# Optimization experiments

Hardware: AMD Instinct MI355X
Metric: run time of the kernel (lower is better)

Reference implementation:

```python
import jax, jax.numpy as jnp
import numpy as np
from jax import lax

B, T, F, C = 2, 249, 64, 256   # fixed by alpha/beta weight shapes in build()
K = 3                          # conv kernel size
FILT = 256                     # q/k conv filters (both blocks)
V = 256                        # v conv filters (both blocks)
OUT_CH = 64                    # conv2d_final filters (hardcoded)


def conv2d(x, w, b):
    # NHWC 'same' conv, stride 1, dilation 1
    return lax.conv_general_dilated(
        x, w, window_strides=(1, 1), padding='SAME',
        dimension_numbers=('NHWC', 'HWIO', 'NHWC')) + b


def attn_block(x, wq, bq, wk, bk, wv, bv):
    # x: [B, H, L, C]; attention over L per (batch, H) slice
    q = conv2d(x, wq, bq)          # [B,H,L,FILT]
    k = conv2d(x, wk, bk)          # [B,H,L,FILT]
    v = conv2d(x, wv, bv)          # [B,H,L,V]
    scores = jnp.einsum('bhqc,bhkc->bhqk', q, k)   # [B,H,L,L]
    dist = jax.nn.softmax(scores, axis=-1)
    return jnp.einsum('bhqk,bhkc->bhqc', dist, v)  # [B,H,L,V]


def setup_inputs() -> dict:
    key = jax.random.key(0)
    ks = jax.random.split(key, 18)
    s = 0.05
    d = {'x': jax.random.normal(ks[0], (B, T, F, C), jnp.float32)}
    names = ['wq_f', 'wk_f', 'wv_f', 'wq_t', 'wk_t', 'wv_t']
    outs = [FILT, FILT, V, FILT, FILT, V]
    for i, (n, o) in enumerate(zip(names, outs)):
        d[n] = jax.random.normal(ks[1 + i], (K, K, C, o), jnp.float32) * s
        d['b' + n[1:]] = jnp.zeros((o,), jnp.float32)
    d['w_final'] = jax.random.normal(ks[8], (K, K, V + V + C, OUT_CH), jnp.float32) * s
    d['b_final'] = jnp.zeros((OUT_CH,), jnp.float32)
    d['alpha'] = jax.random.uniform(ks[9], (B, T, F, V), jnp.float32, -0.05, 0.05)
    d['beta'] = jax.random.uniform(ks[10], (B, T, F, V), jnp.float32, -0.05, 0.05)
    return d


def reference(x, wq_f, bq_f, wk_f, bk_f, wv_f, bv_f,
              wq_t, bq_t, wk_t, bk_t, wv_t, bv_t,
              w_final, b_final, alpha, beta):
    # AFAB: transpose to [B,F,T,C], attend over time axis T
    xt = jnp.transpose(x, (0, 2, 1, 3))
    out_freq = attn_block(xt, wq_f, bq_f, wk_f, bk_f, wv_f, bv_f)
    out_freq = jnp.transpose(out_freq, (0, 2, 1, 3))  # back to [B,T,F,V]
    # ATAB: attend over frequency axis F directly on [B,T,F,C]
    out_time = attn_block(x, wq_t, bq_t, wk_t, bk_t, wv_t, bv_t)
    # learned elementwise gating + concat + final conv (concatenation=True path)
    fused = jnp.concatenate([alpha * out_freq, beta * out_time, x], axis=-1)
    return conv2d(fused, w_final, b_final)
```

## Files before the change

kernel.cpp:

```cpp
#include <hip/hip_runtime.h>


typedef _Float16 f16;
typedef _Float16 f16x8 __attribute__((ext_vector_type(8)));
typedef float    f32x4 __attribute__((ext_vector_type(4)));

#define B_   2
#define T_   249
#define F_   64
#define TP   251
#define FP   66
#define PIXB (T_*F_)
#define NPIX (B_*PIXB)
#define LPAD 256
#define XPOS (B_*TP*FP)

static constexpr size_t FUSED_BYTES = (size_t)B_*TP*FP*768*2;
static constexpr size_t XPAD_BYTES  = (size_t)B_*TP*FP*256*2;
static constexpr size_t QF_BYTES    = (size_t)B_*64*LPAD*256*2;
static constexpr size_t QT_BYTES    = (size_t)B_*T_*64*256*2;
static constexpr size_t WT_BYTES    = (size_t)9*1536*256*2;
static constexpr size_t WFT_BYTES   = (size_t)9*64*768*2;

static constexpr size_t OFF_FUSED = 0;
static constexpr size_t OFF_XPAD  = OFF_FUSED + FUSED_BYTES;
static constexpr size_t OFF_QF    = OFF_XPAD  + XPAD_BYTES;
static constexpr size_t OFF_KF    = OFF_QF + QF_BYTES;
static constexpr size_t OFF_VF    = OFF_KF + QF_BYTES;
static constexpr size_t OFF_QT    = OFF_VF + QF_BYTES;
static constexpr size_t OFF_KT    = OFF_QT + QT_BYTES;
static constexpr size_t OFF_VT    = OFF_KT + QT_BYTES;
static constexpr size_t OFF_WT    = OFF_VT + QT_BYTES;
static constexpr size_t OFF_WFT   = OFF_WT + WT_BYTES;
static constexpr size_t OFF_BALL  = OFF_WFT + WFT_BYTES;
static constexpr size_t OFF_BF    = OFF_BALL + 1536*4;
static constexpr size_t WS_NEED   = OFF_BF + 64*4;

__device__ __forceinline__ f32x4 mfma16(f16x8 a, f16x8 b, f32x4 c) {
    return __builtin_amdgcn_mfma_f32_16x16x32_f16(a, b, c, 0, 0, 0);
}

__device__ __forceinline__ void gl_lds16(const void* g, void* l) {
    __builtin_amdgcn_global_load_lds(
        (const __attribute__((address_space(1))) unsigned int*)(unsigned long long)g,
        (__attribute__((address_space(3))) unsigned int*)(unsigned int)(unsigned long long)l,
        16, 0, 0);
}

__global__ __launch_bounds__(256) void prep_w(
    const float* __restrict__ wqf, const float* __restrict__ wkf, const float* __restrict__ wvf,
    const float* __restrict__ wqt, const float* __restrict__ wkt, const float* __restrict__ wvt,
    const float* __restrict__ wfin,
    const float* __restrict__ bqf, const float* __restrict__ bkf, const float* __restrict__ bvf,
    const float* __restrict__ bqt, const float* __restrict__ bkt, const float* __restrict__ bvt,
    const float* __restrict__ bfin,
    f16* __restrict__ wT, f16* __restrict__ wfT,
    float* __restrict__ biasAll, float* __restrict__ biasF)
{
    int idx = blockIdx.x*256 + threadIdx.x;
    if (idx < 9*1536*256) {
        int tap = idx / (1536*256);
        int r   = idx - tap*(1536*256);
        int n = r >> 8, c = r & 255;
        int dt = tap/3 - 1, df = tap%3 - 1;
        int blk = n >> 8, nl = n & 255;
        const float* w; int kh, kw;
        if (blk < 3) { w = (blk==0) ? wqf : (blk==1) ? wkf : wvf; kh = df+1; kw = dt+1; }
        else         { w = (blk==3) ? wqt : (blk==4) ? wkt : wvt; kh = dt+1; kw = df+1; }
        wT[idx] = (f16)w[((kh*3 + kw)*256 + c)*256 + nl];
    }
    if (idx < 9*64*768) {
        int tap = idx / (64*768);
        int r   = idx - tap*(64*768);
        int oc = r / 768, cin = r - oc*768;
        int dt = tap/3 - 1, df = tap%3 - 1;
        wfT[idx] = (f16)wfin[(((dt+1)*3 + (df+1))*768 + cin)*64 + oc];
    }
    if (idx < 1536) {
        int blk = idx >> 8, nl = idx & 255;
        const float* bb = (blk==0)?bqf:(blk==1)?bkf:(blk==2)?bvf:(blk==3)?bqt:(blk==4)?bkt:bvt;
        biasAll[idx] = bb[nl];
    }
    if (idx < 64) biasF[idx] = bfin[idx];
}

__global__ __launch_bounds__(256) void prep_x(
    const float* __restrict__ x, f16* __restrict__ xpad, f16* __restrict__ fused)
{
    int tid = blockIdx.x*256 + threadIdx.x;
    int pix = tid >> 5, c8 = (tid & 31)*8;
    int b = pix / PIXB; int r = pix - b*PIXB;
    int t = r >> 6, f = r & 63;
    const float* src = x + (size_t)pix*256 + c8;
    f16x8 v;
#pragma unroll
    for (int j = 0; j < 8; ++j) v[j] = (f16)src[j];
    size_t pp = (size_t)(b*TP + t + 1)*FP + (f + 1);
    *(f16x8*)(xpad + pp*256 + c8) = v;
    *(f16x8*)(fused + pp*768 + 512 + c8) = v;
}

__global__ __launch_bounds__(256) void border_zero(
    f16* __restrict__ xpad, f16* __restrict__ fused)
{
    int pix = blockIdx.x*2 + (threadIdx.x >> 7);
    int tl = threadIdx.x & 127;
    int b = pix / 630; int i = pix - b*630;
    int tp, fp;
    if (i < 66)       { tp = 0;   fp = i; }
    else if (i < 132) { tp = 250; fp = i - 66; }
    else { int j = i - 132; tp = 1 + (j >> 1); fp = (j & 1) * 65; }
    size_t pp = (size_t)(b*TP + tp)*FP + fp;
    f16x8 z = {0, 0, 0, 0, 0, 0, 0, 0};
    if (tl < 32) *(f16x8*)(xpad + pp*256 + tl*8) = z;
    if (tl < 96) *(f16x8*)(fused + pp*768 + tl*8) = z;
}

__global__ __launch_bounds__(512, 2) void conv_qkv(
    const f16* __restrict__ xpad, const f16* __restrict__ wT,
    const float* __restrict__ biasAll,
    f16* __restrict__ qf, f16* __restrict__ kf, f16* __restrict__ vf,
    f16* __restrict__ qt, f16* __restrict__ kt_, f16* __restrict__ vt)
{
    __shared__ f16 smemH[448*64];
    __shared__ f16 smemB[2][256*64];

    const int xcd = blockIdx.x & 7, lin = blockIdx.x >> 3;
    const int mtcnt = (xcd < 6) ? 16 : 15;
    if (lin >= 6*mtcnt) return;
    const int mtbase = (xcd < 6) ? xcd*16 : 96 + (xcd - 6)*15;
    const int nt = lin / mtcnt;
    const int mt = mtbase + (lin - nt*mtcnt);

    const int bb_ = mt / 63;
    const int t0  = (mt - bb_*63) * 4;
    const int Gs66 = (bb_*TP + t0) * 66;

    const int l   = threadIdx.x & 63;
    const int wid = threadIdx.x >> 6;
    const int wm = wid >> 2, wn = wid & 3;

    int hOff[7];
#pragma unroll
    for (int j = 0; j < 7; ++j) {
        int pos = j*64 + wid*8 + (l >> 3);
        int ps = pos;
        if (ps > 395) ps = 395;
        int pmax = (XPOS - 1) - Gs66/1;
        { int pm = XPOS - 1 - (bb_*TP + t0)*66; if (ps > pm) ps = pm; }
        (void)pmax;
        int ch = (l & 7) ^ (ps & 7);
        hOff[j] = (Gs66 + ps)*256 + ch*8;
    }
    int bSrc[4];
#pragma unroll
    for (int j = 0; j < 4; ++j) {
        int row = j*64 + wid*8 + (l >> 3);
        int ch = (l & 7) ^ (row & 7);
        bSrc[j] = (nt*256 + row)*256 + ch*8;
    }

    int pos00[8];
#pragma unroll
    for (int m = 0; m < 8; ++m) {
        int r = wm*128 + m*16 + (l & 15);
        pos00[m] = ((r >> 6) + 1)*66 + (r & 63) + 1;
    }
    int bRow[4], bSw[4];
#pragma unroll
    for (int n = 0; n < 4; ++n) {
        int row = wn*64 + n*16 + (l & 15);
        bRow[n] = row*64; bSw[n] = row & 7;
    }

    f32x4 acc[8][4];
#pragma unroll
    for (int m = 0; m < 8; ++m)
#pragma unroll
        for (int n = 0; n < 4; ++n) acc[m][n] = {0.f, 0.f, 0.f, 0.f};

#define HSTAGE(C) do {                                                         \
        _Pragma("unroll")                                                      \
        for (int j_ = 0; j_ < 7; ++j_)                                         \
            gl_lds16(xpad + hOff[j_] + (C)*64,                                 \
                     smemH + (j_*512 + wid*64)*8);                             \
    } while (0)

#define BSTAGE(TAP, C, NB) do {                                                \
        const f16* wt_ = wT + (size_t)(TAP)*(1536*256) + (C)*64;               \
        _Pragma("unroll")                                                      \
        for (int j_ = 0; j_ < 4; ++j_)                                         \
            gl_lds16(wt_ + bSrc[j_], &smemB[NB][(j_*512 + wid*64)*8]);         \
    } while (0)

#define QCOMP(NB, TAPOFF) do {                                                 \
        int pos_[8];                                                           \
        _Pragma("unroll")                                                      \
        for (int m = 0; m < 8; ++m) pos_[m] = pos00[m] + (TAPOFF);             \
        _Pragma("unroll")                                                      \
        for (int kk = 0; kk < 2; ++kk) {                                       \
            const int cch = kk*4 + (l >> 4);                                   \
            f16x8 af[8], bf[4];                                                \
            _Pragma("unroll")                                                  \
            for (int m = 0; m < 8; ++m)                                        \
                af[m] = *(const f16x8*)(smemH + pos_[m]*64 + ((cch ^ (pos_[m] & 7)) << 3)); \
            _Pragma("unroll")                                                  \
            for (int n = 0; n < 4; ++n)                                        \
                bf[n] = *(const f16x8*)(&smemB[NB][0] + bRow[n] + ((cch ^ bSw[n]) << 3)); \
            __builtin_amdgcn_s_setprio(1);                                     \
            _Pragma("unroll")                                                  \
            for (int m = 0; m < 8; ++m)                                        \
                _Pragma("unroll")                                              \
                for (int n = 0; n < 4; ++n)                                    \
                    acc[m][n] = mfma16(af[m], bf[n], acc[m][n]);               \
            __builtin_amdgcn_s_setprio(0);                                     \
        }                                                                      \
    } while (0)

    int buf = 0;
    HSTAGE(0);
    BSTAGE(0, 0, 0);
    __syncthreads();
    for (int c = 0; c < 4; ++c) {
        for (int tap = 0; tap < 9; ++tap) {
            if (tap < 8)      BSTAGE(tap + 1, c, buf ^ 1);
            else if (c < 3)   BSTAGE(0, c + 1, buf ^ 1);
            const int dt = tap/3 - 1, df = tap - (tap/3)*3 - 1;
            QCOMP(buf, dt*66 + df);
            __syncthreads();
            buf ^= 1;
        }
        if (c < 3) {
            HSTAGE(c + 1);
            __syncthreads();
        }
    }
#undef HSTAGE
#undef BSTAGE
#undef QCOMP

    f16* dst = (nt==0)?qf:(nt==1)?kf:(nt==2)?vf:(nt==3)?qt:(nt==4)?kt_:vt;
#pragma unroll
    for (int m = 0; m < 8; ++m) {
#pragma unroll
        for (int rg = 0; rg < 4; ++rg) {
            int row = wm*128 + m*16 + (l >> 4)*4 + rg;
            int t = t0 + (row >> 6), f = row & 63;
            if (t <= 248) {
#pragma unroll
                for (int n = 0; n < 4; ++n) {
                    int col = wn*64 + n*16 + (l & 15);
                    float v = acc[m][n][rg] + biasAll[nt*256 + col];
                    int off;
                    if (nt < 2)       off = ((bb_*64 + f)*LPAD + t)*256 + col;
                    else if (nt == 2) off = ((bb_*64 + f)*256 + col)*LPAD + t;
                    else if (nt < 5)  off = ((bb_*T_ + t)*64 + f)*256 + col;
                    else              off = ((bb_*T_ + t)*256 + col)*64 + f;
                    dst[off] = (f16)v;
                }
            }
        }
    }
}

__global__ __launch_bounds__(256) void attn_f(
    const f16* __restrict__ qf, const f16* __restrict__ kf, const f16* __restrict__ vf,
    const float* __restrict__ alpha, f16* __restrict__ fused)
{
    __shared__ f16 plds[4][16*256];
    const int l = threadIdx.x & 63;
    const int wid = threadIdx.x >> 6;
    const int head = blockIdx.x >> 2;
    const int qb = blockIdx.x & 3;
    const int b = head >> 6, f = head & 63;
    const f16* qh = qf + (size_t)head*LPAD*256;
    const f16* kh = kf + (size_t)head*LPAD*256;
    const f16* vh = vf + (size_t)head*256*LPAD;
    const int qr0 = qb*64 + wid*16;
    f16* pw = &plds[wid][0];

    f16x8 qa[8];
#pragma unroll
    for (int ks = 0; ks < 8; ++ks)
        qa[ks] = *(const f16x8*)(qh + (qr0 + (l & 15))*256 + ks*32 + (l >> 4)*8);

    f32x4 s[16];
#pragma unroll
    for (int nf = 0; nf < 16; ++nf) s[nf] = {0.f, 0.f, 0.f, 0.f};
#pragma unroll
    for (int ks = 0; ks < 8; ++ks)
#pragma unroll
        for (int nf = 0; nf < 16; ++nf) {
            f16x8 bf = *(const f16x8*)(kh + (nf*16 + (l & 15))*256 + ks*32 + (l >> 4)*8);
            s[nf] = mfma16(qa[ks], bf, s[nf]);
        }

    float inv[4];
#pragma unroll
    for (int rg = 0; rg < 4; ++rg) {
        float m = -1e30f;
#pragma unroll
        for (int nf = 0; nf < 16; ++nf)
            if (nf*16 + (l & 15) < T_) m = fmaxf(m, s[nf][rg]);
#pragma unroll
        for (int d = 1; d < 16; d <<= 1) m = fmaxf(m, __shfl_xor(m, d, 64));
        float sum = 0.f;
#pragma unroll
        for (int nf = 0; nf < 16; ++nf) {
            float p = (nf*16 + (l & 15) < T_) ? __expf(s[nf][rg] - m) : 0.f;
            s[nf][rg] = p;
            sum += p;
        }
#pragma unroll
        for (int d = 1; d < 16; d <<= 1) sum += __shfl_xor(sum, d, 64);
        inv[rg] = 1.f / sum;
    }

#pragma unroll
    for (int nf = 0; nf < 16; ++nf)
#pragma unroll
        for (int rg = 0; rg < 4; ++rg) {
            int row = (l >> 4)*4 + rg;
            int col = nf*16 + (l & 15);
            int byte = (row*512 + col*2) ^ ((row & 7) << 4);
            *(f16*)((char*)pw + byte) = (f16)s[nf][rg];
        }

    f32x4 o[16];
#pragma unroll
    for (int nf = 0; nf < 16; ++nf) o[nf] = {0.f, 0.f, 0.f, 0.f};
#pragma unroll
    for (int ks = 0; ks < 8; ++ks) {
        int row = l & 15;
        int cch = ks*4 + (l >> 4);
        int byte = row*512 + ((cch ^ (row & 7)) << 4);
        f16x8 pa = *(const f16x8*)((const char*)pw + byte);
#pragma unroll
        for (int nf = 0; nf < 16; ++nf) {
            f16x8 bf = *(const f16x8*)(vh + (nf*16 + (l & 15))*LPAD + ks*32 + (l >> 4)*8);
            o[nf] = mfma16(pa, bf, o[nf]);
        }
    }

#pragma unroll
    for (int rg = 0; rg < 4; ++rg) {
        int t = qr0 + (l >> 4)*4 + rg;
        if (t < T_) {
#pragma unroll
            for (int nf = 0; nf < 16; ++nf) {
                int c = nf*16 + (l & 15);
                float v = o[nf][rg] * inv[rg] * alpha[((size_t)(b*T_ + t)*64 + f)*256 + c];
                fused[((size_t)(b*TP + t + 1)*FP + (f + 1))*768 + c] = (f16)v;
            }
        }
    }
}

__global__ __launch_bounds__(256) void attn_t(
    const f16* __restrict__ qt, const f16* __restrict__ kt, const f16* __restrict__ vt,
    const float* __restrict__ beta, f16* __restrict__ fused)
{
    __shared__ f16 plds[4][16*64];
    const int l = threadIdx.x & 63;
    const int wid = threadIdx.x >> 6;
    const int head = blockIdx.x;
    const int b = head / T_, t = head - b*T_;
    const f16* qh = qt + (size_t)head*64*256;
    const f16* kh = kt + (size_t)head*64*256;
    const f16* vh = vt + (size_t)head*256*64;
    const int qr0 = wid*16;
    f16* pw = &plds[wid][0];

    f16x8 qa[8];
#pragma unroll
    for (int ks = 0; ks < 8; ++ks)
        qa[ks] = *(const f16x8*)(qh + (qr0 + (l & 15))*256 + ks*32 + (l >> 4)*8);

    f32x4 s[4];
#pragma unroll
    for (int nf = 0; nf < 4; ++nf) s[nf] = {0.f, 0.f, 0.f, 0.f};
#pragma unroll
    for (int ks = 0; ks < 8; ++ks)
#pragma unroll
        for (int nf = 0; nf < 4; ++nf) {
            f16x8 bf = *(const f16x8*)(kh + (nf*16 + (l & 15))*256 + ks*32 + (l >> 4)*8);
            s[nf] = mfma16(qa[ks], bf, s[nf]);
        }

    float inv[4];
#pragma unroll
    for (int rg = 0; rg < 4; ++rg) {
        float m = -1e30f;
#pragma unroll
        for (int nf = 0; nf < 4; ++nf) m = fmaxf(m, s[nf][rg]);
#pragma unroll
        for (int d = 1; d < 16; d <<= 1) m = fmaxf(m, __shfl_xor(m, d, 64));
        float sum = 0.f;
#pragma unroll
        for (int nf = 0; nf < 4; ++nf) {
            float p = __expf(s[nf][rg] - m);
            s[nf][rg] = p;
            sum += p;
        }
#pragma unroll
        for (int d = 1; d < 16; d <<= 1) sum += __shfl_xor(sum, d, 64);
        inv[rg] = 1.f / sum;
    }

#pragma unroll
    for (int nf = 0; nf < 4; ++nf)
#pragma unroll
        for (int rg = 0; rg < 4; ++rg) {
            int row = (l >> 4)*4 + rg;
            int col = nf*16 + (l & 15);
            int byte = (row*128 + col*2) ^ ((row & 7) << 4);
            *(f16*)((char*)pw + byte) = (f16)s[nf][rg];
        }

    f32x4 o[16];
#pragma unroll
    for (int nf = 0; nf < 16; ++nf) o[nf] = {0.f, 0.f, 0.f, 0.f};
#pragma unroll
    for (int ks = 0; ks < 2; ++ks) {
        int row = l & 15;
        int cch = ks*4 + (l >> 4);
        int byte = row*128 + ((cch ^ (row & 7)) << 4);
        f16x8 pa = *(const f16x8*)((const char*)pw + byte);
#pragma unroll
        for (int nf = 0; nf < 16; ++nf) {
            f16x8 bf = *(const f16x8*)(vh + (nf*16 + (l & 15))*64 + ks*32 + (l >> 4)*8);
            o[nf] = mfma16(pa, bf, o[nf]);
        }
    }

#pragma unroll
    for (int rg = 0; rg < 4; ++rg) {
        int fo = qr0 + (l >> 4)*4 + rg;
#pragma unroll
        for (int nf = 0; nf < 16; ++nf) {
            int c = nf*16 + (l & 15);
            float v = o[nf][rg] * inv[rg] * beta[((size_t)(b*T_ + t)*64 + fo)*256 + c];
            fused[((size_t)(b*TP + t + 1)*FP + (fo + 1))*768 + 256 + c] = (f16)v;
        }
    }
}

__global__ __launch_bounds__(256) void conv_final(
    const f16* __restrict__ fused, const f16* __restrict__ wfT,
    const float* __restrict__ biasF, float* __restrict__ out)
{
    __shared__ f16 smem[2][16384];
    const int l = threadIdx.x & 63;
    const int wid = threadIdx.x >> 6;
    const int mt = blockIdx.x;
    const int b = mt / T_, t = mt - b*T_;

    int aSrc[4], bSrc[4];
#pragma unroll
    for (int i = 0; i < 4; ++i) {
        int row = i*16 + wid*4 + (l >> 4);
        int ch  = (l & 15) ^ (row & 7);
        aSrc[i] = ((b*TP + t + 1)*FP + (row + 1))*768 + ch*8;
        bSrc[i] = row*768 + ch*8;
    }

    int aRowOff, aSwz;
    { int row = wid*16 + (l & 15); aRowOff = row*128; aSwz = row & 7; }
    int bRow[4], bSw[4];
#pragma unroll
    for (int ni = 0; ni < 4; ++ni) {
        int row = ni*16 + (l & 15);
        bRow[ni] = 8192 + row*128; bSw[ni] = row & 7;
    }

    f32x4 acc[4];
#pragma unroll
    for (int ni = 0; ni < 4; ++ni) acc[ni] = {0.f, 0.f, 0.f, 0.f};

#define FSTAGE(KN, NB) do {                                                    \
        int tap_ = (KN) / 6, kc_ = (KN) - ((KN)/6)*6;                          \
        int ash_ = ((tap_/3 - 1)*FP + (tap_%3 - 1))*768 + kc_*128;             \
        const f16* wt_ = wfT + (size_t)tap_*(64*768) + kc_*128;                \
        _Pragma("unroll")                                                      \
        for (int i_ = 0; i_ < 4; ++i_) {                                       \
            gl_lds16(fused + aSrc[i_] + ash_, &smem[NB][(i_*16 + wid*4)*128]); \
            gl_lds16(wt_ + bSrc[i_], &smem[NB][8192 + (i_*16 + wid*4)*128]);   \
        }                                                                      \
    } while (0)

#define FCOMP(NB) do {                                                         \
        _Pragma("unroll")                                                      \
        for (int kk = 0; kk < 4; ++kk) {                                       \
            const int cch = kk*4 + (l >> 4);                                   \
            f16x8 af = *(const f16x8*)(&smem[NB][0] + aRowOff + ((cch ^ aSwz) << 3)); \
            f16x8 bf[4];                                                       \
            _Pragma("unroll")                                                  \
            for (int ni = 0; ni < 4; ++ni)                                     \
                bf[ni] = *(const f16x8*)(&smem[NB][0] + bRow[ni] + ((cch ^ bSw[ni]) << 3)); \
            __builtin_amdgcn_s_setprio(1);                                     \
            _Pragma("unroll")                                                  \
            for (int ni = 0; ni < 4; ++ni)                                     \
                acc[ni] = mfma16(af, bf[ni], acc[ni]);                         \
            __builtin_amdgcn_s_setprio(0);                                     \
        }                                                                      \
    } while (0)

    FSTAGE(0, 0);
    __syncthreads();
    for (int kn = 0; kn < 54; kn += 2) {
        if (kn + 1 < 54) FSTAGE(kn + 1, 1);
        FCOMP(0);
        __syncthreads();
        if (kn + 2 < 54) FSTAGE(kn + 2, 0);
        FCOMP(1);
        __syncthreads();
    }
#undef FSTAGE
#undef FCOMP

#pragma unroll
    for (int rg = 0; rg < 4; ++rg) {
        int f = wid*16 + (l >> 4)*4 + rg;
        int p = mt*64 + f;
#pragma unroll
        for (int ni = 0; ni < 4; ++ni) {
            int oc = ni*16 + (l & 15);
            out[(size_t)p*64 + oc] = acc[ni][rg] + biasF[oc];
        }
    }
}

extern "C" void kernel_launch(void* const* d_in, const int* in_sizes, int n_in,
                              void* d_out, int out_size, void* d_ws, size_t ws_size,
                              hipStream_t stream) {
    (void)in_sizes; (void)n_in; (void)out_size;
    const float* x    = (const float*)d_in[0];
    const float* wqf  = (const float*)d_in[1];
    const float* bqf  = (const float*)d_in[2];
    const float* wkf  = (const float*)d_in[3];
    const float* bkf  = (const float*)d_in[4];
    const float* wvf  = (const float*)d_in[5];
    const float* bvf  = (const float*)d_in[6];
    const float* wqt  = (const float*)d_in[7];
    const float* bqt  = (const float*)d_in[8];
    const float* wkt  = (const float*)d_in[9];
    const float* bkt  = (const float*)d_in[10];
    const float* wvt  = (const float*)d_in[11];
    const float* bvt  = (const float*)d_in[12];
    const float* wfin = (const float*)d_in[13];
    const float* bfin = (const float*)d_in[14];
    const float* alpha= (const float*)d_in[15];
    const float* beta = (const float*)d_in[16];

    if (ws_size < WS_NEED) return;

    char* ws = (char*)d_ws;
    f16* fused  = (f16*)(ws + OFF_FUSED);
    f16* xpad   = (f16*)(ws + OFF_XPAD);
    f16* qf     = (f16*)(ws + OFF_QF);
    f16* kf     = (f16*)(ws + OFF_KF);
    f16* vf     = (f16*)(ws + OFF_VF);
    f16* qt     = (f16*)(ws + OFF_QT);
    f16* kt     = (f16*)(ws + OFF_KT);
    f16* vt     = (f16*)(ws + OFF_VT);
    f16* wT     = (f16*)(ws + OFF_WT);
    f16* wfT    = (f16*)(ws + OFF_WFT);
    float* bAll = (float*)(ws + OFF_BALL);
    float* bF   = (float*)(ws + OFF_BF);

    hipMemsetAsync(vf, 0, QF_BYTES, stream);

    border_zero<<<dim3(630), dim3(256), 0, stream>>>(xpad, fused);
    prep_w<<<dim3((9*1536*256 + 255)/256), dim3(256), 0, stream>>>(
        wqf, wkf, wvf, wqt, wkt, wvt, wfin,
        bqf, bkf, bvf, bqt, bkt, bvt, bfin, wT, wfT, bAll, bF);
    prep_x<<<dim3(NPIX*32/256), dim3(256), 0, stream>>>(x, xpad, fused);
    conv_qkv<<<dim3(768), dim3(512), 0, stream>>>(xpad, wT, bAll, qf, kf, vf, qt, kt, vt);
    attn_f<<<dim3(512), dim3(256), 0, stream>>>(qf, kf, vf, alpha, fused);
    attn_t<<<dim3(498), dim3(256), 0, stream>>>(qt, kt, vt, beta, fused);
    conv_final<<<dim3(498), dim3(256), 0, stream>>>(fused, wfT, bF, (float*)d_out);
}
```

Measured before the change: 496.2 us.

## Restructure final conv to reuse a shared halo tile across all nine taps

The final 3x3 conv now gives each block two time rows (128 pixels) and loads a halo tile of 288 positions by 64 channels into shared memory once per channel chunk. All nine taps then read that tile at shifted offsets, while only the weight slices are double-buffered per tap. This replaces the old scheme, which reloaded the shifted activation tile from global memory for every tap. The cost is 250 blocks instead of 498 (lower occupancy and parallelism on the GPU), more synchronisation points, and a halo load that is not overlapped with compute.

```diff
diff --git a/kernel.cpp b/kernel.cpp
--- a/kernel.cpp
+++ b/kernel.cpp
@@ -146,9 +146,7 @@
         int pos = j*64 + wid*8 + (l >> 3);
         int ps = pos;
         if (ps > 395) ps = 395;
-        int pmax = (XPOS - 1) - Gs66/1;
         { int pm = XPOS - 1 - (bb_*TP + t0)*66; if (ps > pm) ps = pm; }
-        (void)pmax;
         int ch = (l & 7) ^ (ps & 7);
         hOff[j] = (Gs66 + ps)*256 + ch*8;
     }
@@ -445,87 +443,133 @@
     }
 }
 
-__global__ __launch_bounds__(256) void conv_final(
+__global__ __launch_bounds__(256, 2) void conv_final(
     const f16* __restrict__ fused, const f16* __restrict__ wfT,
     const float* __restrict__ biasF, float* __restrict__ out)
 {
-    __shared__ f16 smem[2][16384];
-    const int l = threadIdx.x & 63;
-    const int wid = threadIdx.x >> 6;
+    __shared__ f16 smemH[288*64];
+    __shared__ f16 smemB[2][64*64];
+
     const int mt = blockIdx.x;
-    const int b = mt / T_, t = mt - b*T_;
-
-    int aSrc[4], bSrc[4];
-#pragma unroll
-    for (int i = 0; i < 4; ++i) {
-        int row = i*16 + wid*4 + (l >> 4);
-        int ch  = (l & 15) ^ (row & 7);
-        aSrc[i] = ((b*TP + t + 1)*FP + (row + 1))*768 + ch*8;
-        bSrc[i] = row*768 + ch*8;
-    }
-
-    int aRowOff, aSwz;
-    { int row = wid*16 + (l & 15); aRowOff = row*128; aSwz = row & 7; }
-    int bRow[4], bSw[4];
-#pragma unroll
-    for (int ni = 0; ni < 4; ++ni) {
-        int row = ni*16 + (l & 15);
-        bRow[ni] = 8192 + row*128; bSw[ni] = row & 7;
-    }
-
-    f32x4 acc[4];
-#pragma unroll
-    for (int ni = 0; ni < 4; ++ni) acc[ni] = {0.f, 0.f, 0.f, 0.f};
-
-#define FSTAGE(KN, NB) do {                                                    \
-        int tap_ = (KN) / 6, kc_ = (KN) - ((KN)/6)*6;                          \
-        int ash_ = ((tap_/3 - 1)*FP + (tap_%3 - 1))*768 + kc_*128;             \
-        const f16* wt_ = wfT + (size_t)tap_*(64*768) + kc_*128;                \
-        _Pragma("unroll")                                                      \
-        for (int i_ = 0; i_ < 4; ++i_) {                                       \
-            gl_lds16(fused + aSrc[i_] + ash_, &smem[NB][(i_*16 + wid*4)*128]); \
-            gl_lds16(wt_ + bSrc[i_], &smem[NB][8192 + (i_*16 + wid*4)*128]);   \
-        }                                                                      \
+    const int bb = mt / 125;
+    const int t0 = (mt - bb*125) * 2;
+    const int Gs66 = (bb*TP + t0) * 66;
+
+    const int tid = threadIdx.x;
+    const int l   = tid & 63;
+    const int wid = tid >> 6;
+    const int wm = wid >> 1, wn = wid & 1;
+
+    int hOff[9];
+#pragma unroll
+    for (int j = 0; j < 9; ++j) {
+        int ps = j*32 + (tid >> 3);
+        if (ps > 263) ps = 263;
+        { int pm = XPOS - 1 - (bb*TP + t0)*66; if (ps > pm) ps = pm; }
+        int ch = (tid & 7) ^ (ps & 7);
+        hOff[j] = (Gs66 + ps)*768 + ch*8;
+    }
+    int bSrc[2];
+#pragma unroll
+    for (int j = 0; j < 2; ++j) {
+        int row = j*32 + (tid >> 3);
+        int ch  = (tid & 7) ^ (row & 7);
+        bSrc[j] = row*768 + ch*8;
+    }
+
+    int pos00[4];
+#pragma unroll
+    for (int m = 0; m < 4; ++m) {
+        int r = wm*64 + m*16 + (l & 15);
+        pos00[m] = ((r >> 6) + 1)*66 + (r & 63) + 1;
+    }
+    int bRow[2], bSw[2];
+#pragma unroll
+    for (int n = 0; n < 2; ++n) {
+        int row = wn*32 + n*16 + (l & 15);
+        bRow[n] = row*64; bSw[n] = row & 7;
+    }
+
+    f32x4 acc[4][2];
+#pragma unroll
+    for (int m = 0; m < 4; ++m)
+#pragma unroll
+        for (int n = 0; n < 2; ++n) acc[m][n] = {0.f, 0.f, 0.f, 0.f};
+
+#define FHSTAGE(C) do {                                                        \
+        _Pragma("unroll")                                                      \
+        for (int j_ = 0; j_ < 9; ++j_)                                         \
+            gl_lds16(fused + hOff[j_] + (C)*64,                                \
+                     smemH + (j_*256 + wid*64)*8);                             \
     } while (0)
 
-#define FCOMP(NB) do {                                                         \
-        _Pragma("unroll")                                                      \
-        for (int kk = 0; kk < 4; ++kk) {                                       \
+#define FBSTAGE(TAP, C, NB) do {                                               \
+        const f16* wt_ = wfT + (size_t)(TAP)*(64*768) + (C)*64;                \
+        _Pragma("unroll")                                                      \
+        for (int j_ = 0; j_ < 2; ++j_)                                         \
+            gl_lds16(wt_ + bSrc[j_], &smemB[NB][(j_*256 + wid*64)*8]);         \
+    } while (0)
+
+#define FCOMP(NB, TAPOFF) do {                                                 \
+        int pos_[4];                                                           \
+        _Pragma("unroll")                                                      \
+        for (int m = 0; m < 4; ++m) pos_[m] = pos00[m] + (TAPOFF);             \
+        _Pragma("unroll")                                                      \
+        for (int kk = 0; kk < 2; ++kk) {                                       \
             const int cch = kk*4 + (l >> 4);                                   \
-            f16x8 af = *(const f16x8*)(&smem[NB][0] + aRowOff + ((cch ^ aSwz) << 3)); \
-            f16x8 bf[4];                                                       \
+            f16x8 af[4], bf[2];                                                \
             _Pragma("unroll")                                                  \
-            for (int ni = 0; ni < 4; ++ni)                                     \
-                bf[ni] = *(const f16x8*)(&smem[NB][0] + bRow[ni] + ((cch ^ bSw[ni]) << 3)); \
+            for (int m = 0; m < 4; ++m)                                        \
+                af[m] = *(const f16x8*)(smemH + pos_[m]*64 + ((cch ^ (pos_[m] & 7)) << 3)); \
+            _Pragma("unroll")                                                  \
+            for (int n = 0; n < 2; ++n)                                        \
+                bf[n] = *(const f16x8*)(&smemB[NB][0] + bRow[n] + ((cch ^ bSw[n]) << 3)); \
             __builtin_amdgcn_s_setprio(1);                                     \
             _Pragma("unroll")                                                  \
-            for (int ni = 0; ni < 4; ++ni)                                     \
-                acc[ni] = mfma16(af, bf[ni], acc[ni]);                         \
+            for (int m = 0; m < 4; ++m)                                        \
+                _Pragma("unroll")                                              \
+                for (int n = 0; n < 2; ++n)                                    \
+                    acc[m][n] = mfma16(af[m], bf[n], acc[m][n]);               \
             __builtin_amdgcn_s_setprio(0);                                     \
         }                                                                      \
     } while (0)
 
-    FSTAGE(0, 0);
+    int buf = 0;
+    FHSTAGE(0);
+    FBSTAGE(0, 0, 0);
     __syncthreads();
-    for (int kn = 0; kn < 54; kn += 2) {
-        if (kn + 1 < 54) FSTAGE(kn + 1, 1);
-        FCOMP(0);
-        __syncthreads();
-        if (kn + 2 < 54) FSTAGE(kn + 2, 0);
-        FCOMP(1);
-        __syncthreads();
-    }
-#undef FSTAGE
+    for (int c = 0; c < 12; ++c) {
+        for (int tap = 0; tap < 9; ++tap) {
+            if (tap < 8)       FBSTAGE(tap + 1, c, buf ^ 1);
+            else if (c < 11)   FBSTAGE(0, c + 1, buf ^ 1);
+            const int dt = tap/3 - 1, df = tap - (tap/3)*3 - 1;
+            FCOMP(buf, dt*66 + df);
+            __syncthreads();
+            buf ^= 1;
+        }
+        if (c < 11) {
+            FHSTAGE(c + 1);
+            __syncthreads();
+        }
+    }
+#undef FHSTAGE
+#undef FBSTAGE
 #undef FCOMP
 
 #pragma unroll
-    for (int rg = 0; rg < 4; ++rg) {
-        int f = wid*16 + (l >> 4)*4 + rg;
-        int p = mt*64 + f;
-#pragma unroll
-        for (int ni = 0; ni < 4; ++ni) {
-            int oc = ni*16 + (l & 15);
-            out[(size_t)p*64 + oc] = acc[ni][rg] + biasF[oc];
+    for (int m = 0; m < 4; ++m) {
+#pragma unroll
+        for (int rg = 0; rg < 4; ++rg) {
+            int r = wm*64 + m*16 + (l >> 4)*4 + rg;
+            int t = t0 + (r >> 6), f = r & 63;
+            if (t <= 248) {
+                size_t pix = (size_t)bb*PIXB + t*64 + f;
+#pragma unroll
+                for (int n = 0; n < 2; ++n) {
+                    int oc = wn*32 + n*16 + (l & 15);
+                    out[pix*64 + oc] = acc[m][n][rg] + biasF[oc];
+                }
+            }
         }
     }
 }
@@ -578,5 +622,5 @@
     conv_qkv<<<dim3(768), dim3(512), 0, stream>>>(xpad, wT, bAll, qf, kf, vf, qt, kt, vt);
     attn_f<<<dim3(512), dim3(256), 0, stream>>>(qf, kf, vf, alpha, fused);
     attn_t<<<dim3(498), dim3(256), 0, stream>>>(qt, kt, vt, beta, fused);
-    conv_final<<<dim3(498), dim3(256), 0, stream>>>(fused, wfT, bF, (float*)d_out);
-}
+    conv_final<<<dim3(250), dim3(256), 0, stream>>>(fused, wfT, bF, (float*)d_out);
+}
```

Result: no change. 502.2 us (+1.2%).
